# Kernel optimization log

Hardware: AMD Instinct MI355X
Metric: run time of the kernel (lower is better)

Reference implementation:

```python
import jax, jax.numpy as jnp
import numpy as np


def setup_inputs() -> dict:
    key = jax.random.key(0)
    k1, k2, k3, k4 = jax.random.split(key, 4)
    B, V, P, C, R, N, OUT = 8, 4096, 32, 32, 2, 16, 32  # N=(l_max+1)^2, l_max=3
    signal = jax.random.normal(k1, (B, V, C), dtype=jnp.float32)
    patches_idx = jax.random.randint(k2, (B, V, P), 0, V, dtype=jnp.int32)
    conv_kernel = jax.random.normal(k3, (B, V, P, R, N), dtype=jnp.float32)
    kernel_weights = jax.random.normal(k4, (OUT, C, R, N), dtype=jnp.float32) * 0.05
    biases = jnp.zeros((OUT,), dtype=jnp.float32)
    return {
        "signal": signal,
        "patches_idx": patches_idx,
        "conv_kernel": conv_kernel,
        "kernel_weights": kernel_weights,
        "biases": biases,
    }


def reference(signal, patches_idx, conv_kernel, kernel_weights, biases):
    # Gather per-vertex tree-neighbor patches (tf.gather_nd with batch idx):
    # signal [B,V,C], patches_idx [B,V,P] -> patches [B,V,P,C]
    patches = jax.vmap(lambda s, i: s[i])(signal, patches_idx)
    # Bilinear contraction with precomputed SH conv kernel: [B,V,P,R,N] x [B,V,P,C]
    y = jnp.einsum('bvprn,bvpc->bvcrn', conv_kernel, patches)
    # Learned weights contraction: [OUT,C,R,N] x [B,V,C,R,N] -> [B,V,OUT]
    y = jnp.einsum('ijrn,bvjrn->bvi', kernel_weights, y)
    y = y + biases
    return jax.nn.relu(y)
```

## Files before the change

kernel.cpp:

```cpp
#include <hip/hip_runtime.h>


typedef __attribute__((ext_vector_type(8))) short bf16x8;
typedef __attribute__((ext_vector_type(16))) float f32x16;
typedef __attribute__((ext_vector_type(4))) float f32x4;

__device__ __forceinline__ unsigned short f2bf_rne(float f) {
    union { float f; unsigned int u; } x;
    x.f = f;
    unsigned int u = x.u;
    return (unsigned short)((u + 0x7fffu + ((u >> 16) & 1u)) >> 16);
}
__device__ __forceinline__ unsigned short f2bf_rh(float f) {
    union { float f; unsigned int u; } x;
    x.f = f;
    return (unsigned short)((x.u + 0x8000u) >> 16);
}

__global__ __launch_bounds__(256) void prep_kernel(
        const float* __restrict__ W, const float* __restrict__ sig,
        unsigned short* __restrict__ Wf, unsigned short* __restrict__ sigbf) {
    int tid = blockIdx.x * 256 + threadIdx.x;
    if (tid < 32768) {
        int j = tid & 7;
        int l = (tid >> 3) & 63;
        int pair = tid >> 9;
        int s = pair >> 1;
        int t = pair & 1;
        int i = 16 * t + (l & 15);
        int crn = 32 * s + 8 * (l >> 4) + j;
        Wf[tid] = f2bf_rne(W[i * 1024 + crn]);
    } else {
        int e = (tid - 32768) * 8;
        if (e < 8 * 4096 * 32) {
            f32x4 a = *(const f32x4*)(sig + e);
            f32x4 b = *(const f32x4*)(sig + e + 4);
            bf16x8 v;
            v[0] = (short)f2bf_rne(a[0]); v[1] = (short)f2bf_rne(a[1]);
            v[2] = (short)f2bf_rne(a[2]); v[3] = (short)f2bf_rne(a[3]);
            v[4] = (short)f2bf_rne(b[0]); v[5] = (short)f2bf_rne(b[1]);
            v[6] = (short)f2bf_rne(b[2]); v[7] = (short)f2bf_rne(b[3]);
            *(bf16x8*)(sigbf + e) = v;
        }
    }
}

__global__ __launch_bounds__(256, 4) void fused_kernel(
        const unsigned short* __restrict__ sigbf, const int* __restrict__ pidx,
        const float* __restrict__ ck, const unsigned short* __restrict__ Wf,
        const float* __restrict__ bias, float* __restrict__ out) {
    __shared__ __align__(16) unsigned short T_lds[16 * 1032];
    const int tid = threadIdx.x;
    const int l = tid & 63;
    const int w = tid >> 6;
    const int m0 = blockIdx.x * 16;
    const int b = m0 >> 12;
    const int cc = l & 31;
    const int g = l >> 5;
    const unsigned short* sgb = sigbf + (size_t)b * (4096 * 32);
    const unsigned short* ckh = (const unsigned short*)ck;

    auto load_q = [&](int q, unsigned short (&sa)[16], unsigned short (&kb)[16]) {
        const int m = m0 + w * 4 + q;
        const int* idxp = pidx + (size_t)m * 32;
        const size_t kh = ((size_t)m * 1024) * 2 + 1;
        #pragma unroll
        for (int h = 0; h < 2; ++h) {
            #pragma unroll
            for (int j = 0; j < 8; ++j) {
                const int p = h * 16 + 8 * g + j;
                sa[h * 8 + j] = sgb[idxp[p] * 32 + cc];
                kb[h * 8 + j] = ckh[kh + (size_t)(p * 32 + cc) * 2];
            }
        }
    };
    auto compute_q = [&](int q, const unsigned short (&sa)[16],
                         const unsigned short (&kb)[16]) {
        f32x16 acc = {};
        #pragma unroll
        for (int h = 0; h < 2; ++h) {
            bf16x8 af, bfr;
            #pragma unroll
            for (int j = 0; j < 8; ++j) {
                af[j]  = (short)sa[h * 8 + j];
                bfr[j] = (short)kb[h * 8 + j];
            }
            acc = __builtin_amdgcn_mfma_f32_32x32x16_bf16(af, bfr, acc, 0, 0, 0);
        }
        unsigned short* trow = T_lds + (w * 4 + q) * 1032 + cc + g * 128;
        #pragma unroll
        for (int r = 0; r < 16; ++r)
            trow[((r & 3) + 8 * (r >> 2)) * 32] = f2bf_rh(acc[r]);
    };

    unsigned short a0[16], k0[16], a1[16], k1[16];
    load_q(0, a0, k0);
    load_q(1, a1, k1);
    compute_q(0, a0, k0); load_q(2, a0, k0);
    compute_q(1, a1, k1); load_q(3, a1, k1);
    compute_q(2, a0, k0);
    compute_q(3, a1, k1);

    bf16x8 wfa[8], wfb[8];
    #pragma unroll
    for (int si = 0; si < 8; ++si) {
        const int s = 8 * w + si;
        const bf16x8* wrow = (const bf16x8*)(Wf + (size_t)(s * 2) * 512);
        wfa[si] = wrow[l];
        wfb[si] = wrow[64 + l];
    }
    __syncthreads();

    f32x4 acc0 = {}, acc1 = {};
    const int lg = l >> 4;
    const int ln = l & 15;
    #pragma unroll
    for (int si = 0; si < 8; ++si) {
        const int s = 8 * w + si;
        const bf16x8 af = *(const bf16x8*)(T_lds + ln * 1032 + s * 32 + 8 * lg);
        acc0 = __builtin_amdgcn_mfma_f32_16x16x32_bf16(af, wfa[si], acc0, 0, 0, 0);
        acc1 = __builtin_amdgcn_mfma_f32_16x16x32_bf16(af, wfb[si], acc1, 0, 0, 0);
    }
    __syncthreads();

    float* red = (float*)T_lds;
    {
        f32x4* rp = (f32x4*)(red + w * 512);
        rp[l]      = acc0;
        rp[64 + l] = acc1;
    }
    __syncthreads();

    #pragma unroll
    for (int o0 = 0; o0 < 2; ++o0) {
        const int o = o0 * 256 + tid;
        float sum = red[o] + red[512 + o] + red[1024 + o] + red[1536 + o];
        const int t  = o >> 8;
        const int ll = (o >> 2) & 63;
        const int r  = o & 3;
        const int bv = ((ll >> 4) << 2) + r;
        const int i  = 16 * t + (ll & 15);
        sum += bias[i];
        out[(size_t)(m0 + bv) * 32 + i] = sum > 0.f ? sum : 0.f;
    }
}

extern "C" void kernel_launch(void* const* d_in, const int* in_sizes, int n_in,
                              void* d_out, int out_size, void* d_ws, size_t ws_size,
                              hipStream_t stream) {
    const float* sig  = (const float*)d_in[0];
    const int*   pidx = (const int*)d_in[1];
    const float* ck   = (const float*)d_in[2];
    const float* W    = (const float*)d_in[3];
    const float* bias = (const float*)d_in[4];
    float* out = (float*)d_out;
    unsigned short* Wf    = (unsigned short*)d_ws;
    unsigned short* sigbf = Wf + 32768;

    prep_kernel<<<640, 256, 0, stream>>>(W, sig, Wf, sigbf);
    fused_kernel<<<2048, 256, 0, stream>>>(sigbf, pidx, ck, Wf, bias, out);
}
```

Baseline: 42.55 us.

## Materialize gathered bf16 patches in prep kernel and drop manual load pipelining

The prep kernel now performs the neighbor gather, writing a bf16 patch tensor [B,V,P,C] to workspace, so the fused kernel reads contiguous patches instead of indirectly indexing signal through pidx. The hand-written double-buffered load/compute schedule is replaced by a simple loop. This trades a 64MB-class intermediate write plus read (about 2M*32 bf16 = 64MB write, then read) for removing dependent index loads in the main kernel, and it may lose latency hiding.

```diff
diff --git a/kernel.cpp b/kernel.cpp
--- a/kernel.cpp
+++ b/kernel.cpp
@@ -19,87 +19,71 @@
 
 __global__ __launch_bounds__(256) void prep_kernel(
         const float* __restrict__ W, const float* __restrict__ sig,
-        unsigned short* __restrict__ Wf, unsigned short* __restrict__ sigbf) {
-    int tid = blockIdx.x * 256 + threadIdx.x;
-    if (tid < 32768) {
+        const int* __restrict__ pidx,
+        unsigned short* __restrict__ Wf, unsigned short* __restrict__ pat) {
+    if (blockIdx.x < 16384) {
+        const int t = blockIdx.x * 256 + threadIdx.x;
+        const int bvp = t >> 2;
+        const int c0 = (t & 3) * 8;
+        const int row = pidx[bvp];
+        const int b = bvp >> 17;
+        const float* src = sig + ((size_t)(b << 12) + row) * 32 + c0;
+        f32x4 a = *(const f32x4*)src;
+        f32x4 d = *(const f32x4*)(src + 4);
+        bf16x8 v;
+        v[0] = (short)f2bf_rne(a[0]); v[1] = (short)f2bf_rne(a[1]);
+        v[2] = (short)f2bf_rne(a[2]); v[3] = (short)f2bf_rne(a[3]);
+        v[4] = (short)f2bf_rne(d[0]); v[5] = (short)f2bf_rne(d[1]);
+        v[6] = (short)f2bf_rne(d[2]); v[7] = (short)f2bf_rne(d[3]);
+        *(bf16x8*)(pat + (size_t)bvp * 32 + c0) = v;
+    } else {
+        const int tid = (blockIdx.x - 16384) * 256 + threadIdx.x;
         int j = tid & 7;
         int l = (tid >> 3) & 63;
         int pair = tid >> 9;
         int s = pair >> 1;
-        int t = pair & 1;
-        int i = 16 * t + (l & 15);
+        int t2 = pair & 1;
+        int i = 16 * t2 + (l & 15);
         int crn = 32 * s + 8 * (l >> 4) + j;
         Wf[tid] = f2bf_rne(W[i * 1024 + crn]);
-    } else {
-        int e = (tid - 32768) * 8;
-        if (e < 8 * 4096 * 32) {
-            f32x4 a = *(const f32x4*)(sig + e);
-            f32x4 b = *(const f32x4*)(sig + e + 4);
-            bf16x8 v;
-            v[0] = (short)f2bf_rne(a[0]); v[1] = (short)f2bf_rne(a[1]);
-            v[2] = (short)f2bf_rne(a[2]); v[3] = (short)f2bf_rne(a[3]);
-            v[4] = (short)f2bf_rne(b[0]); v[5] = (short)f2bf_rne(b[1]);
-            v[6] = (short)f2bf_rne(b[2]); v[7] = (short)f2bf_rne(b[3]);
-            *(bf16x8*)(sigbf + e) = v;
-        }
     }
 }
 
 __global__ __launch_bounds__(256, 4) void fused_kernel(
-        const unsigned short* __restrict__ sigbf, const int* __restrict__ pidx,
-        const float* __restrict__ ck, const unsigned short* __restrict__ Wf,
-        const float* __restrict__ bias, float* __restrict__ out) {
+        const unsigned short* __restrict__ pat, const float* __restrict__ ck,
+        const unsigned short* __restrict__ Wf, const float* __restrict__ bias,
+        float* __restrict__ out) {
     __shared__ __align__(16) unsigned short T_lds[16 * 1032];
     const int tid = threadIdx.x;
     const int l = tid & 63;
     const int w = tid >> 6;
     const int m0 = blockIdx.x * 16;
-    const int b = m0 >> 12;
     const int cc = l & 31;
     const int g = l >> 5;
-    const unsigned short* sgb = sigbf + (size_t)b * (4096 * 32);
     const unsigned short* ckh = (const unsigned short*)ck;
 
-    auto load_q = [&](int q, unsigned short (&sa)[16], unsigned short (&kb)[16]) {
-        const int m = m0 + w * 4 + q;
-        const int* idxp = pidx + (size_t)m * 32;
+    for (int q = 0; q < 4; ++q) {
+        const int bvl = w * 4 + q;
+        const int m = m0 + bvl;
+        const unsigned short* pb = pat + (size_t)m * 1024;
         const size_t kh = ((size_t)m * 1024) * 2 + 1;
-        #pragma unroll
-        for (int h = 0; h < 2; ++h) {
-            #pragma unroll
-            for (int j = 0; j < 8; ++j) {
-                const int p = h * 16 + 8 * g + j;
-                sa[h * 8 + j] = sgb[idxp[p] * 32 + cc];
-                kb[h * 8 + j] = ckh[kh + (size_t)(p * 32 + cc) * 2];
-            }
-        }
-    };
-    auto compute_q = [&](int q, const unsigned short (&sa)[16],
-                         const unsigned short (&kb)[16]) {
         f32x16 acc = {};
         #pragma unroll
         for (int h = 0; h < 2; ++h) {
             bf16x8 af, bfr;
             #pragma unroll
             for (int j = 0; j < 8; ++j) {
-                af[j]  = (short)sa[h * 8 + j];
-                bfr[j] = (short)kb[h * 8 + j];
+                const int p = h * 16 + 8 * g + j;
+                af[j]  = (short)pb[p * 32 + cc];
+                bfr[j] = (short)ckh[kh + (size_t)(p * 32 + cc) * 2];
             }
             acc = __builtin_amdgcn_mfma_f32_32x32x16_bf16(af, bfr, acc, 0, 0, 0);
         }
-        unsigned short* trow = T_lds + (w * 4 + q) * 1032 + cc + g * 128;
+        unsigned short* trow = T_lds + bvl * 1032 + cc + g * 128;
         #pragma unroll
         for (int r = 0; r < 16; ++r)
             trow[((r & 3) + 8 * (r >> 2)) * 32] = f2bf_rh(acc[r]);
-    };
-
-    unsigned short a0[16], k0[16], a1[16], k1[16];
-    load_q(0, a0, k0);
-    load_q(1, a1, k1);
-    compute_q(0, a0, k0); load_q(2, a0, k0);
-    compute_q(1, a1, k1); load_q(3, a1, k1);
-    compute_q(2, a0, k0);
-    compute_q(3, a1, k1);
+    }
 
     bf16x8 wfa[8], wfb[8];
     #pragma unroll
@@ -154,9 +138,9 @@
     const float* W    = (const float*)d_in[3];
     const float* bias = (const float*)d_in[4];
     float* out = (float*)d_out;
-    unsigned short* Wf    = (unsigned short*)d_ws;
-    unsigned short* sigbf = Wf + 32768;
+    unsigned short* Wf  = (unsigned short*)d_ws;
+    unsigned short* pat = Wf + 32768;
 
-    prep_kernel<<<640, 256, 0, stream>>>(W, sig, Wf, sigbf);
-    fused_kernel<<<2048, 256, 0, stream>>>(sigbf, pidx, ck, Wf, bias, out);
+    prep_kernel<<<16512, 256, 0, stream>>>(W, sig, pidx, Wf, pat);
+    fused_kernel<<<2048, 256, 0, stream>>>(pat, ck, Wf, bias, out);
 }
```

Measured after the change: 53.48 us. 1.26x slower.
